# Kernel optimization log

Hardware: AMD Instinct MI355X
Metric: run time of the kernel (lower is better)

The kernel has to match this reference:

```python
import jax, jax.numpy as jnp
import numpy as np
import math

B, D, C = 256, 512, 100000
SCALE = 64.0
MARGIN = 0.5
ALPHA = 1.2
SIGMA = 2.0
THRESH = math.cos(math.pi - MARGIN)
MM = math.sin(math.pi - MARGIN) * MARGIN


def _l2_normalize(x, axis=-1, eps=1e-12):
    n = jnp.linalg.norm(x, axis=axis, keepdims=True)
    return x / jnp.maximum(n, eps)


def setup_inputs() -> dict:
    key = jax.random.key(0)
    k1, k2, k3 = jax.random.split(key, 3)
    inp = jax.random.normal(k1, (B, D), dtype=jnp.float32)
    label = jax.random.randint(k2, (B,), 0, C, dtype=jnp.int64)
    stdv = 1.0 / math.sqrt(D)
    weight = jax.random.uniform(k3, (C, D), dtype=jnp.float32, minval=-stdv, maxval=stdv)
    return {"input": inp, "label": label, "weight": weight}


def reference(input, label, weight):
    # cosine similarity: [B, C]
    cos = _l2_normalize(input) @ _l2_normalize(weight).T
    rows = jnp.arange(cos.shape[0])
    cos_lb = cos[rows, label]  # [B]
    # angular margin on the target logit, with the standard arcface fallback
    a_lb = jnp.where(
        cos_lb > THRESH,
        jnp.cos(jnp.arccos(jnp.clip(cos_lb, -1.0, 1.0)) + MARGIN),
        cos_lb - MM,
    )  # [B]
    # gaussian reweighting of negatives around the margined target logit (detached)
    t_scale = jax.lax.stop_gradient(
        ALPHA * jnp.exp(-jnp.square(cos - a_lb[:, None]) / SIGMA)
    )  # [B, C]
    onehot = jax.nn.one_hot(label, cos.shape[1], dtype=cos.dtype)  # [B, C]
    logits = SCALE * (
        onehot * a_lb[:, None] + (1.0 - onehot) * (t_scale * cos + t_scale - 1.0)
    )
    return logits
```

## Files before the change

kernel.cpp:

```cpp
#include <hip/hip_runtime.h>
#include <hip/hip_bf16.h>
#include <math.h>

#define B_ 256
#define D_ 512
#define C_ 100000

#define SCALE_  64.0f
#define ALPHA_  1.2f
#define THRESH_ (-0.8775825618903728f)
#define MM_     (0.23971276930210156f)
#define COSM_   (0.8775825618903728f)
#define SINM_   (0.4794255386042030f)

typedef __bf16 bf16x8 __attribute__((ext_vector_type(8)));
typedef __bf16 bf16x4 __attribute__((ext_vector_type(4)));
typedef float  f32x4  __attribute__((ext_vector_type(4)));

__global__ void prep_kernel(const float* __restrict__ inp,
                            const int* __restrict__ lab_raw,
                            const float* __restrict__ weight,
                            __bf16* __restrict__ xn,
                            float* __restrict__ a_lb,
                            int* __restrict__ lab32) {
    const int b = blockIdx.x;
    const int l = threadIdx.x;

    const bool is64 = (lab_raw[1] == 0) & (lab_raw[3] == 0) & (lab_raw[5] == 0) &
                      (lab_raw[7] == 0) & (lab_raw[9] == 0) & (lab_raw[11] == 0) &
                      (lab_raw[13] == 0) & (lab_raw[15] == 0);
    const int lab = is64 ? lab_raw[2 * b] : lab_raw[b];

    const float* ip = inp + b * D_ + l * 8;
    f32x4 v0 = *(const f32x4*)ip;
    f32x4 v1 = *(const f32x4*)(ip + 4);
    float ss = v0.x * v0.x + v0.y * v0.y + v0.z * v0.z + v0.w * v0.w +
               v1.x * v1.x + v1.y * v1.y + v1.z * v1.z + v1.w * v1.w;
#pragma unroll
    for (int m = 1; m < 64; m <<= 1) ss += __shfl_xor(ss, m);
    const float ninv = 1.0f / fmaxf(sqrtf(ss), 1e-12f);

    float xf[8] = {v0.x * ninv, v0.y * ninv, v0.z * ninv, v0.w * ninv,
                   v1.x * ninv, v1.y * ninv, v1.z * ninv, v1.w * ninv};
    bf16x8 xv;
#pragma unroll
    for (int i = 0; i < 8; ++i) xv[i] = (__bf16)xf[i];
    *(bf16x8*)(xn + b * D_ + l * 8) = xv;

    const float* wp = weight + (size_t)lab * D_ + l * 8;
    f32x4 w0 = *(const f32x4*)wp;
    f32x4 w1 = *(const f32x4*)(wp + 4);
    float wss = w0.x * w0.x + w0.y * w0.y + w0.z * w0.z + w0.w * w0.w +
                w1.x * w1.x + w1.y * w1.y + w1.z * w1.z + w1.w * w1.w;
    float dp = xf[0] * w0.x + xf[1] * w0.y + xf[2] * w0.z + xf[3] * w0.w +
               xf[4] * w1.x + xf[5] * w1.y + xf[6] * w1.z + xf[7] * w1.w;
#pragma unroll
    for (int m = 1; m < 64; m <<= 1) {
        wss += __shfl_xor(wss, m);
        dp  += __shfl_xor(dp, m);
    }
    if (l == 0) {
        const float cos_lb = dp / fmaxf(sqrtf(wss), 1e-12f);
        const float ccl = fminf(fmaxf(cos_lb, -1.0f), 1.0f);
        const float s = sqrtf(fmaxf(0.0f, 1.0f - ccl * ccl));
        const float a1 = ccl * COSM_ - s * SINM_;
        a_lb[b] = (cos_lb > THRESH_) ? a1 : (cos_lb - MM_);
        lab32[b] = lab;
    }
}

#define BN 128
#define BK 64

__global__ __launch_bounds__(512)
void gemm_kernel(const __bf16* __restrict__ xn,
                 const float* __restrict__ weight,
                 const float* __restrict__ a_lb,
                 const int* __restrict__ lab32,
                 float* __restrict__ out) {
    __shared__ __align__(16) char aT[B_ * BK * 2];
    __shared__ __align__(16) char wT[BN * BK * 2];
    __shared__ float wssq[BN];

    const int tid  = threadIdx.x;
    const int lane = tid & 63;
    const int wid  = tid >> 6;
    const int wm   = wid >> 1;
    const int wn   = wid & 1;
    const int n0   = blockIdx.x * BN;

    f32x4 acc[4][4] = {};
    float wss[4] = {0.f, 0.f, 0.f, 0.f};

    const int wrow = tid >> 4;
    const int wc4  = (tid & 15) * 4;
    const int arow = tid >> 3;
    const int acg  = (tid & 7) * 8;

    for (int kt = 0; kt < D_ / BK; ++kt) {
        const int k0 = kt * BK;
        __syncthreads();
#pragma unroll
        for (int r = 0; r < 4; ++r) {
            const int row = arow + r * 64;
            uint4 v = *(const uint4*)(xn + row * D_ + k0 + acg);
            int off = (row * BK + acg) * 2;
            off ^= (row & 7) << 4;
            *(uint4*)(aT + off) = v;
        }
#pragma unroll
        for (int r = 0; r < 4; ++r) {
            const int row = wrow + r * 32;
            int g = n0 + row;
            g = (g < C_) ? g : (C_ - 1);
            f32x4 v = *(const f32x4*)(weight + (size_t)g * D_ + k0 + wc4);
            wss[r] += v.x * v.x + v.y * v.y + v.z * v.z + v.w * v.w;
            bf16x4 h;
            h[0] = (__bf16)v.x; h[1] = (__bf16)v.y;
            h[2] = (__bf16)v.z; h[3] = (__bf16)v.w;
            int off = (row * BK + wc4) * 2;
            off ^= (row & 7) << 4;
            *(bf16x4*)(wT + off) = h;
        }
        __syncthreads();

        const int lr = lane & 15;
        const int lk = (lane >> 4) * 8;
#pragma unroll
        for (int ks = 0; ks < 2; ++ks) {
            bf16x8 af[4], bfr[4];
#pragma unroll
            for (int m = 0; m < 4; ++m) {
                const int row = wm * 64 + m * 16 + lr;
                int off = (row * BK + ks * 32 + lk) * 2;
                off ^= (row & 7) << 4;
                af[m] = *(const bf16x8*)(aT + off);
            }
#pragma unroll
            for (int n = 0; n < 4; ++n) {
                const int row = wn * 64 + n * 16 + lr;
                int off = (row * BK + ks * 32 + lk) * 2;
                off ^= (row & 7) << 4;
                bfr[n] = *(const bf16x8*)(wT + off);
            }
#pragma unroll
            for (int m = 0; m < 4; ++m)
#pragma unroll
                for (int n = 0; n < 4; ++n)
                    acc[m][n] = __builtin_amdgcn_mfma_f32_16x16x32_bf16(
                        af[m], bfr[n], acc[m][n], 0, 0, 0);
        }
    }

#pragma unroll
    for (int r = 0; r < 4; ++r) {
        float s = wss[r];
        s += __shfl_xor(s, 1);
        s += __shfl_xor(s, 2);
        s += __shfl_xor(s, 4);
        s += __shfl_xor(s, 8);
        if ((tid & 15) == 0) wssq[wrow + r * 32] = s;
    }
    __syncthreads();

    float al_r[16];
    int   lb_r[16];
    const int rb0 = wm * 64 + ((lane >> 4) << 2);
#pragma unroll
    for (int m = 0; m < 4; ++m)
#pragma unroll
        for (int j = 0; j < 4; ++j) {
            const int b = rb0 + m * 16 + j;
            al_r[m * 4 + j] = a_lb[b];
            lb_r[m * 4 + j] = lab32[b];
        }

#pragma unroll
    for (int n = 0; n < 4; ++n) {
        const int ln = wn * 64 + n * 16 + (lane & 15);
        const int c = n0 + ln;
        const float winv = 1.0f / fmaxf(sqrtf(wssq[ln]), 1e-12f);
        const bool ok = (c < C_);
#pragma unroll
        for (int m = 0; m < 4; ++m)
#pragma unroll
            for (int j = 0; j < 4; ++j) {
                const int b = rb0 + m * 16 + j;
                const float al = al_r[m * 4 + j];
                const float cosv = acc[m][n][j] * winv;
                const float d = cosv - al;
                const float t = ALPHA_ * __expf(-0.5f * d * d);
                const float o = (c == lb_r[m * 4 + j]) ? al : (t * cosv + t - 1.0f);
                if (ok) out[(size_t)b * C_ + c] = SCALE_ * o;
            }
    }
}

extern "C" void kernel_launch(void* const* d_in, const int* in_sizes, int n_in,
                              void* d_out, int out_size, void* d_ws, size_t ws_size,
                              hipStream_t stream) {
    const float* inp = (const float*)d_in[0];
    const int*   lab = (const int*)d_in[1];
    const float* w   = (const float*)d_in[2];
    float* out = (float*)d_out;

    char* ws = (char*)d_ws;
    __bf16* xn   = (__bf16*)ws;
    float*  a_lb = (float*)(ws + 262144);
    int*    l32  = (int*)(ws + 262144 + 1024);

    prep_kernel<<<B_, 64, 0, stream>>>(inp, lab, w, xn, a_lb, l32);
    gemm_kernel<<<(C_ + BN - 1) / BN, 512, 0, stream>>>(xn, w, a_lb, l32, out);
}
```

Baseline: 103.9 us.

## Pre-swizzle normalized input into MFMA fragment layout and read A from global

```diff
diff --git a/kernel.cpp b/kernel.cpp
--- a/kernel.cpp
+++ b/kernel.cpp
@@ -20,7 +20,7 @@
 __global__ void prep_kernel(const float* __restrict__ inp,
                             const int* __restrict__ lab_raw,
                             const float* __restrict__ weight,
-                            __bf16* __restrict__ xn,
+                            __bf16* __restrict__ xnf,
                             float* __restrict__ a_lb,
                             int* __restrict__ lab32) {
     const int b = blockIdx.x;
@@ -45,7 +45,10 @@
     bf16x8 xv;
 #pragma unroll
     for (int i = 0; i < 8; ++i) xv[i] = (__bf16)xf[i];
-    *(bf16x8*)(xn + b * D_ + l * 8) = xv;
+
+    const int tile_idx = (b >> 4) * 16 + (l >> 2);
+    const int lf = (b & 15) + ((l & 3) << 4);
+    *(bf16x8*)((char*)xnf + tile_idx * 1024 + lf * 16) = xv;
 
     const float* wp = weight + (size_t)lab * D_ + l * 8;
     f32x4 w0 = *(const f32x4*)wp;
@@ -69,77 +72,83 @@
     }
 }
 
-#define BN 128
+#define BN 64
 #define BK 64
 
-__global__ __launch_bounds__(512)
-void gemm_kernel(const __bf16* __restrict__ xn,
+__global__ __launch_bounds__(256, 3)
+void gemm_kernel(const __bf16* __restrict__ xnf,
                  const float* __restrict__ weight,
                  const float* __restrict__ a_lb,
                  const int* __restrict__ lab32,
                  float* __restrict__ out) {
-    __shared__ __align__(16) char aT[B_ * BK * 2];
     __shared__ __align__(16) char wT[BN * BK * 2];
     __shared__ float wssq[BN];
 
     const int tid  = threadIdx.x;
     const int lane = tid & 63;
-    const int wid  = tid >> 6;
-    const int wm   = wid >> 1;
-    const int wn   = wid & 1;
+    const int wm   = tid >> 6;
     const int n0   = blockIdx.x * BN;
 
     f32x4 acc[4][4] = {};
-    float wss[4] = {0.f, 0.f, 0.f, 0.f};
-
-    const int wrow = tid >> 4;
-    const int wc4  = (tid & 15) * 4;
-    const int arow = tid >> 3;
-    const int acg  = (tid & 7) * 8;
+    float wss = 0.0f;
+
+    const int wrow = tid >> 2;
+    const int wc   = (tid & 3) * 16;
+    int grow = n0 + wrow;
+    grow = (grow < C_) ? grow : (C_ - 1);
+    const float* wbase = weight + (size_t)grow * D_ + wc;
+
+    f32x4 wpre[4];
+#pragma unroll
+    for (int i = 0; i < 4; ++i) wpre[i] = *(const f32x4*)(wbase + i * 4);
 
     for (int kt = 0; kt < D_ / BK; ++kt) {
-        const int k0 = kt * BK;
+        if (kt) __syncthreads();
+        bf16x8 h0, h1;
+#pragma unroll
+        for (int i = 0; i < 4; ++i) {
+            f32x4 v = wpre[i];
+            wss += v.x * v.x + v.y * v.y + v.z * v.z + v.w * v.w;
+            if (i < 2) {
+                h0[i * 4 + 0] = (__bf16)v.x; h0[i * 4 + 1] = (__bf16)v.y;
+                h0[i * 4 + 2] = (__bf16)v.z; h0[i * 4 + 3] = (__bf16)v.w;
+            } else {
+                h1[(i - 2) * 4 + 0] = (__bf16)v.x; h1[(i - 2) * 4 + 1] = (__bf16)v.y;
+                h1[(i - 2) * 4 + 2] = (__bf16)v.z; h1[(i - 2) * 4 + 3] = (__bf16)v.w;
+            }
+        }
+        {
+            int off0 = wrow * (BK * 2) + wc * 2;
+            int off1 = off0 + 16;
+            off0 ^= (wrow & 7) << 4;
+            off1 ^= (wrow & 7) << 4;
+            *(bf16x8*)(wT + off0) = h0;
+            *(bf16x8*)(wT + off1) = h1;
+        }
         __syncthreads();
-#pragma unroll
-        for (int r = 0; r < 4; ++r) {
-            const int row = arow + r * 64;
-            uint4 v = *(const uint4*)(xn + row * D_ + k0 + acg);
-            int off = (row * BK + acg) * 2;
-            off ^= (row & 7) << 4;
-            *(uint4*)(aT + off) = v;
-        }
-#pragma unroll
-        for (int r = 0; r < 4; ++r) {
-            const int row = wrow + r * 32;
-            int g = n0 + row;
-            g = (g < C_) ? g : (C_ - 1);
-            f32x4 v = *(const f32x4*)(weight + (size_t)g * D_ + k0 + wc4);
-            wss[r] += v.x * v.x + v.y * v.y + v.z * v.z + v.w * v.w;
-            bf16x4 h;
-            h[0] = (__bf16)v.x; h[1] = (__bf16)v.y;
-            h[2] = (__bf16)v.z; h[3] = (__bf16)v.w;
-            int off = (row * BK + wc4) * 2;
-            off ^= (row & 7) << 4;
-            *(bf16x4*)(wT + off) = h;
-        }
-        __syncthreads();
-
-        const int lr = lane & 15;
-        const int lk = (lane >> 4) * 8;
+
+        if (kt < D_ / BK - 1) {
+            const float* p = wbase + (kt + 1) * BK;
+#pragma unroll
+            for (int i = 0; i < 4; ++i) wpre[i] = *(const f32x4*)(p + i * 4);
+        }
+
+        bf16x8 af[2][4];
+#pragma unroll
+        for (int ks = 0; ks < 2; ++ks)
+#pragma unroll
+            for (int m = 0; m < 4; ++m) {
+                const int tile = (wm * 4 + m) * 16 + kt * 2 + ks;
+                af[ks][m] = *(const bf16x8*)((const char*)xnf + tile * 1024 + lane * 16);
+            }
+
 #pragma unroll
         for (int ks = 0; ks < 2; ++ks) {
-            bf16x8 af[4], bfr[4];
-#pragma unroll
-            for (int m = 0; m < 4; ++m) {
-                const int row = wm * 64 + m * 16 + lr;
-                int off = (row * BK + ks * 32 + lk) * 2;
-                off ^= (row & 7) << 4;
-                af[m] = *(const bf16x8*)(aT + off);
-            }
+            bf16x8 bfr[4];
 #pragma unroll
             for (int n = 0; n < 4; ++n) {
-                const int row = wn * 64 + n * 16 + lr;
-                int off = (row * BK + ks * 32 + lk) * 2;
+                const int row = n * 16 + (lane & 15);
+                int off = row * (BK * 2) + ks * 64 + (lane >> 4) * 16;
                 off ^= (row & 7) << 4;
                 bfr[n] = *(const bf16x8*)(wT + off);
             }
@@ -148,18 +157,15 @@
 #pragma unroll
                 for (int n = 0; n < 4; ++n)
                     acc[m][n] = __builtin_amdgcn_mfma_f32_16x16x32_bf16(
-                        af[m], bfr[n], acc[m][n], 0, 0, 0);
-        }
-    }
-
-#pragma unroll
-    for (int r = 0; r < 4; ++r) {
-        float s = wss[r];
+                        af[ks][m], bfr[n], acc[m][n], 0, 0, 0);
+        }
+    }
+
+    {
+        float s = wss;
         s += __shfl_xor(s, 1);
         s += __shfl_xor(s, 2);
-        s += __shfl_xor(s, 4);
-        s += __shfl_xor(s, 8);
-        if ((tid & 15) == 0) wssq[wrow + r * 32] = s;
+        if ((tid & 3) == 0) wssq[wrow] = s;
     }
     __syncthreads();
 
@@ -177,7 +183,7 @@
 
 #pragma unroll
     for (int n = 0; n < 4; ++n) {
-        const int ln = wn * 64 + n * 16 + (lane & 15);
+        const int ln = n * 16 + (lane & 15);
         const int c = n0 + ln;
         const float winv = 1.0f / fmaxf(sqrtf(wssq[ln]), 1e-12f);
         const bool ok = (c < C_);
@@ -205,10 +211,10 @@
     float* out = (float*)d_out;
 
     char* ws = (char*)d_ws;
-    __bf16* xn   = (__bf16*)ws;
+    __bf16* xnf  = (__bf16*)ws;
     float*  a_lb = (float*)(ws + 262144);
     int*    l32  = (int*)(ws + 262144 + 1024);
 
-    prep_kernel<<<B_, 64, 0, stream>>>(inp, lab, w, xn, a_lb, l32);
-    gemm_kernel<<<(C_ + BN - 1) / BN, 512, 0, stream>>>(xn, w, a_lb, l32, out);
+    prep_kernel<<<B_, 64, 0, stream>>>(inp, lab, w, xnf, a_lb, l32);
+    gemm_kernel<<<(C_ + BN - 1) / BN, 256, 0, stream>>>(xnf, w, a_lb, l32, out);
 }
```

Result: faster. 88.88 us (-14.4%).
